# Performance work log

Measured on AMD Instinct MI355X. Metric: run time of the kernel, lower is better.

Reference implementation:

```python
import jax, jax.numpy as jnp
import numpy as np

INPUT_DIM, DIM_K, DIM_V = 1024, 512, 512

def setup_inputs() -> dict:
    key = jax.random.key(0)
    kx, kq, kk, kv = jax.random.split(key, 4)
    x = jax.random.normal(kx, (4, 4096, INPUT_DIM), dtype=jnp.float32)
    s = 1.0 / np.sqrt(INPUT_DIM)
    Wq = jax.random.normal(kq, (INPUT_DIM, DIM_K), dtype=jnp.float32) * s
    Wk = jax.random.normal(kk, (INPUT_DIM, DIM_K), dtype=jnp.float32) * s
    Wv = jax.random.normal(kv, (INPUT_DIM, DIM_V), dtype=jnp.float32) * s
    return {"x": x, "Wq": Wq, "Wk": Wk, "Wv": Wv}

def reference(x, Wq, Wk, Wv):
    # x: [b, n, d_in]; bias-free projections
    Q = jnp.einsum('bnd,dk->bnk', x, Wq)
    K = jnp.einsum('bnd,dk->bnk', x, Wk)
    V = jnp.einsum('bnd,dv->bnv', x, Wv)
    scale = 1.0 / np.sqrt(Wq.shape[1])
    scores = jnp.einsum('bqk,bnk->bqn', Q, K) * scale  # [b, n, n]
    atten = jax.nn.softmax(scores, axis=-1)
    return jnp.einsum('bqn,bnv->bqv', atten, V)
```

## Files before the change

kernel.cpp:

```cpp
#include <hip/hip_runtime.h>
#include <hip/hip_bf16.h>


typedef __attribute__((ext_vector_type(8))) short bf16x8;
typedef __attribute__((ext_vector_type(4))) float floatx4;

static __device__ __forceinline__ unsigned short f2bf(float f) {
    unsigned int u = __builtin_bit_cast(unsigned int, f);
    return (unsigned short)((u + 0x7fffu + ((u >> 16) & 1u)) >> 16);
}

static __device__ __forceinline__ void gl2lds16(const unsigned short* g, unsigned short* l) {
    __builtin_amdgcn_global_load_lds(
        (const __attribute__((address_space(1))) unsigned int*)g,
        (__attribute__((address_space(3))) unsigned int*)l, 16, 0, 0);
}

__global__ __launch_bounds__(256) void cvt_bf16(const float* __restrict__ X,
                                                unsigned short* __restrict__ Y, int n4) {
    int i = blockIdx.x * 256 + threadIdx.x;
    if (i < n4) {
        float4 v = reinterpret_cast<const float4*>(X)[i];
        ushort4 o;
        o.x = f2bf(v.x); o.y = f2bf(v.y); o.z = f2bf(v.z); o.w = f2bf(v.w);
        reinterpret_cast<ushort4*>(Y)[i] = o;
    }
}

__global__ __launch_bounds__(256) void transpose_w(const float* __restrict__ W,
                                                   unsigned short* __restrict__ Wt) {
    __shared__ float tile[32][33];
    int n0 = blockIdx.x * 32;
    int k0 = blockIdx.y * 32;
    int tx = threadIdx.x & 31, ty = threadIdx.x >> 5;
    for (int i = 0; i < 32; i += 8)
        tile[ty + i][tx] = W[(size_t)(k0 + ty + i) * 512 + n0 + tx];
    __syncthreads();
    for (int i = 0; i < 32; i += 8)
        Wt[(size_t)(n0 + ty + i) * 1024 + k0 + tx] = f2bf(tile[tx][ty + i]);
}

template <int MODE>
__global__ __launch_bounds__(256) void gemm_bt(const unsigned short* __restrict__ A,
                                               const unsigned short* __restrict__ Bt,
                                               unsigned short* __restrict__ C,
                                               int M, int N, int K) {
    __shared__ unsigned short As[128 * 32];
    __shared__ unsigned short Bs[128 * 32];
    const int m0 = blockIdx.y * 128, n0 = blockIdx.x * 128;
    const int tid = threadIdx.x;
    const int lane = tid & 63, wave = tid >> 6;
    const int wm = (wave >> 1) * 64, wn = (wave & 1) * 64;
    const int quad = lane >> 4, l15 = lane & 15;

    floatx4 acc[4][4] = {};
    const int srow = tid >> 2, scol = (tid & 3) * 8;

    for (int kt = 0; kt < K; kt += 32) {
        const unsigned short* ga = A + (size_t)(m0 + srow) * K + kt + scol;
        const unsigned short* gb = Bt + (size_t)(n0 + srow) * K + kt + scol;
        gl2lds16(ga, As + tid * 8);
        gl2lds16(ga + (size_t)64 * K, As + 2048 + tid * 8);
        gl2lds16(gb, Bs + tid * 8);
        gl2lds16(gb + (size_t)64 * K, Bs + 2048 + tid * 8);
        __syncthreads();
        bf16x8 af[4], bfr[4];
#pragma unroll
        for (int i = 0; i < 4; i++)
            af[i] = *reinterpret_cast<const bf16x8*>(As + (wm + i * 16 + l15) * 32 + quad * 8);
#pragma unroll
        for (int j = 0; j < 4; j++)
            bfr[j] = *reinterpret_cast<const bf16x8*>(Bs + (wn + j * 16 + l15) * 32 + quad * 8);
#pragma unroll
        for (int i = 0; i < 4; i++)
#pragma unroll
            for (int j = 0; j < 4; j++)
                acc[i][j] = __builtin_amdgcn_mfma_f32_16x16x32_bf16(af[i], bfr[j], acc[i][j], 0, 0, 0);
        __syncthreads();
    }

    const float qscale = 0.044194173824159216f;
#pragma unroll
    for (int i = 0; i < 4; i++)
#pragma unroll
        for (int j = 0; j < 4; j++)
#pragma unroll
            for (int r = 0; r < 4; r++) {
                int row = m0 + wm + i * 16 + quad * 4 + r;
                int col = n0 + wn + j * 16 + l15;
                float val = (MODE == 0) ? acc[i][j][r] * qscale : acc[i][j][r];
                unsigned short v = f2bf(val);
                if (MODE == 0) {
                    C[(size_t)row * N + col] = v;
                } else if (MODE == 1) {
                    size_t base = ((size_t)((row >> 12) * 128 + ((row & 4095) >> 5))) << 14;
                    int off = ((col >> 5) * 2 + ((row >> 4) & 1)) * 512 +
                              (((col >> 3) & 3) * 16 + (row & 15)) * 8 + (col & 7);
                    C[base + off] = v;
                } else {
                    size_t base = ((size_t)((col >> 12) * 128 + ((col & 4095) >> 5))) << 14;
                    int off = (row >> 4) * 512 +
                              (((col >> 3) & 3) * 16 + (row & 15)) * 8 + (col & 7);
                    C[base + off] = v;
                }
            }
}

__global__ __launch_bounds__(256, 2) void attn(const unsigned short* __restrict__ Qg,
                                               const unsigned short* __restrict__ Kf,
                                               const unsigned short* __restrict__ Vf,
                                               float* __restrict__ O0,
                                               float* __restrict__ O1,
                                               float* __restrict__ lpart) {
    __shared__ unsigned short Kb[16384];
    __shared__ unsigned short Vb[16384];
    __shared__ unsigned short Ps[4][512];

    const int b = blockIdx.y;
    const int q0 = blockIdx.x * 64;
    const int h = blockIdx.z;
    const int tid = threadIdx.x;
    const int lane = tid & 63, wave = tid >> 6;
    const int quad = lane >> 4, l15 = lane & 15;

    const unsigned short* KfB = Kf + ((size_t)b << 21);
    const unsigned short* VfB = Vf + ((size_t)b << 21);
    float* Od = (h == 0) ? O0 : O1;

    bf16x8 qf[16];
    {
        const unsigned short* qrow =
            Qg + (size_t)(b * 4096 + q0 + wave * 16 + l15) * 512 + quad * 8;
#pragma unroll
        for (int ks = 0; ks < 16; ks++)
            qf[ks] = *reinterpret_cast<const bf16x8*>(qrow + ks * 32);
    }

    floatx4 o[4][8];
#pragma unroll
    for (int g = 0; g < 4; g++)
#pragma unroll
        for (int n2 = 0; n2 < 8; n2++) o[g][n2] = floatx4{0.f, 0.f, 0.f, 0.f};
    float lp[4] = {0.f, 0.f, 0.f, 0.f};

    const int kt0 = h * 64;
    for (int kt = kt0; kt < kt0 + 64; kt++) {
        const unsigned short* gK = KfB + ((size_t)kt << 14);
        const unsigned short* gV = VfB + ((size_t)kt << 14);
#pragma unroll
        for (int i = 0; i < 8; i++)
            gl2lds16(gK + (i * 256 + tid) * 8, &Kb[(i * 256 + tid) * 8]);
#pragma unroll
        for (int i = 0; i < 8; i++)
            gl2lds16(gV + (i * 256 + tid) * 8, &Vb[(i * 256 + tid) * 8]);
        __syncthreads();

        floatx4 s00 = {0.f,0.f,0.f,0.f}, s01 = {0.f,0.f,0.f,0.f};
        floatx4 s10 = {0.f,0.f,0.f,0.f}, s11 = {0.f,0.f,0.f,0.f};
#pragma unroll
        for (int ks = 0; ks < 16; ks += 2) {
            bf16x8 k0a = *reinterpret_cast<const bf16x8*>(Kb + (2 * ks + 0) * 512 + lane * 8);
            bf16x8 k1a = *reinterpret_cast<const bf16x8*>(Kb + (2 * ks + 1) * 512 + lane * 8);
            bf16x8 k0b = *reinterpret_cast<const bf16x8*>(Kb + (2 * ks + 2) * 512 + lane * 8);
            bf16x8 k1b = *reinterpret_cast<const bf16x8*>(Kb + (2 * ks + 3) * 512 + lane * 8);
            s00 = __builtin_amdgcn_mfma_f32_16x16x32_bf16(qf[ks], k0a, s00, 0, 0, 0);
            s10 = __builtin_amdgcn_mfma_f32_16x16x32_bf16(qf[ks], k1a, s10, 0, 0, 0);
            s01 = __builtin_amdgcn_mfma_f32_16x16x32_bf16(qf[ks + 1], k0b, s01, 0, 0, 0);
            s11 = __builtin_amdgcn_mfma_f32_16x16x32_bf16(qf[ks + 1], k1b, s11, 0, 0, 0);
        }
        floatx4 s0v = s00 + s01, s1v = s10 + s11;

        unsigned short* Pw = &Ps[wave][0];
#pragma unroll
        for (int r = 0; r < 4; r++) {
            float p0 = __expf(s0v[r] - 16.0f);
            float p1 = __expf(s1v[r] - 16.0f);
            lp[r] += p0 + p1;
            int row = quad * 4 + r;
            Pw[(l15 >> 3) * 128 + row * 8 + (l15 & 7)] = f2bf(p0);
            Pw[((l15 >> 3) + 2) * 128 + row * 8 + (l15 & 7)] = f2bf(p1);
        }
        __syncthreads();

        bf16x8 vfr[8];
#pragma unroll
        for (int n2 = 0; n2 < 8; n2++)
            vfr[n2] = *reinterpret_cast<const bf16x8*>(Vb + (wave * 8 + n2) * 512 + lane * 8);
#pragma unroll
        for (int g = 0; g < 4; g++) {
            bf16x8 pf = *reinterpret_cast<const bf16x8*>(&Ps[g][0] + lane * 8);
#pragma unroll
            for (int n2 = 0; n2 < 8; n2++)
                o[g][n2] = __builtin_amdgcn_mfma_f32_16x16x32_bf16(pf, vfr[n2], o[g][n2], 0, 0, 0);
        }
        __syncthreads();
    }

#pragma unroll
    for (int off = 1; off < 16; off <<= 1)
#pragma unroll
        for (int r = 0; r < 4; r++) lp[r] += __shfl_xor(lp[r], off);
    if (l15 == 0) {
#pragma unroll
        for (int r = 0; r < 4; r++)
            lpart[h * 16384 + b * 4096 + q0 + wave * 16 + quad * 4 + r] = lp[r];
    }

#pragma unroll
    for (int g = 0; g < 4; g++)
#pragma unroll
        for (int r = 0; r < 4; r++) {
            size_t rowoff = (size_t)(b * 4096 + q0 + g * 16 + quad * 4 + r) * 512 + wave * 128 + l15;
#pragma unroll
            for (int n2 = 0; n2 < 8; n2++)
                Od[rowoff + n2 * 16] = o[g][n2][r];
        }
}

__global__ __launch_bounds__(256) void combine(float* __restrict__ Out,
                                               const float* __restrict__ O1,
                                               const float* __restrict__ lpart) {
    int i = blockIdx.x * 256 + threadIdx.x;
    int row = i >> 7;
    float inv = 1.0f / (lpart[row] + lpart[16384 + row]);
    float4 a = reinterpret_cast<const float4*>(Out)[i];
    float4 c = reinterpret_cast<const float4*>(O1)[i];
    float4 r;
    r.x = (a.x + c.x) * inv;
    r.y = (a.y + c.y) * inv;
    r.z = (a.z + c.z) * inv;
    r.w = (a.w + c.w) * inv;
    reinterpret_cast<float4*>(Out)[i] = r;
}

extern "C" void kernel_launch(void* const* d_in, const int* in_sizes, int n_in,
                              void* d_out, int out_size, void* d_ws, size_t ws_size,
                              hipStream_t stream) {
    const float* x  = (const float*)d_in[0];
    const float* Wq = (const float*)d_in[1];
    const float* Wk = (const float*)d_in[2];
    const float* Wv = (const float*)d_in[3];

    char* ws = (char*)d_ws;
    unsigned short* Wqt = (unsigned short*)(ws);
    unsigned short* Wkt = (unsigned short*)(ws + (1u << 20));
    unsigned short* Wvt = (unsigned short*)(ws + (2u << 20));
    unsigned short* Qb  = (unsigned short*)(ws + (3u << 20));
    unsigned short* Kfr = (unsigned short*)(ws + (19u << 20));
    unsigned short* Vfr = (unsigned short*)(ws + (35u << 20));
    unsigned short* xb  = (unsigned short*)(ws + (51u << 20));
    float* O1    = (float*)(ws + (51u << 20));
    float* lpart = (float*)(ws + (83u << 20));

    dim3 tb(256);
    cvt_bf16<<<dim3(16384), tb, 0, stream>>>(x, xb, 16384 * 1024 / 4);
    transpose_w<<<dim3(16, 32), tb, 0, stream>>>(Wq, Wqt);
    transpose_w<<<dim3(16, 32), tb, 0, stream>>>(Wk, Wkt);
    transpose_w<<<dim3(16, 32), tb, 0, stream>>>(Wv, Wvt);
    gemm_bt<0><<<dim3(4, 128), tb, 0, stream>>>(xb, Wqt, Qb, 16384, 512, 1024);
    gemm_bt<1><<<dim3(4, 128), tb, 0, stream>>>(xb, Wkt, Kfr, 16384, 512, 1024);
    gemm_bt<2><<<dim3(128, 4), tb, 0, stream>>>(Wvt, xb, Vfr, 512, 16384, 1024);
    attn<<<dim3(64, 4, 2), tb, 0, stream>>>(Qb, Kfr, Vfr, (float*)d_out, O1, lpart);
    combine<<<dim3(8192), tb, 0, stream>>>((float*)d_out, O1, lpart);
}
```

Baseline: 373.3 us.

## Fuse QKV projections into one GEMM and double-buffer attention K/V tiles

The three projection GEMMs are merged into a single launch over a concatenated transposed weight, and each block writes Q, K-fragment or V-fragment layout depending on its column range. V is now produced in the non-transposed orientation with a recomputed fragment index. The attention kernel grows to 512 threads covering 128 queries, with two query halves sharing each K/V tile, and double-buffers K/V in LDS using async loads with explicit vmcnt waits and raw barriers so the next tile's load overlaps current compute. This roughly doubles LDS use per block, which may limit occupancy, and the hand-written waitcnt counts are fragile. It also issues one redundant wrapped prefetch on the last iteration.

```diff
diff --git a/kernel.cpp b/kernel.cpp
--- a/kernel.cpp
+++ b/kernel.cpp
@@ -15,6 +15,12 @@
         (const __attribute__((address_space(1))) unsigned int*)g,
         (__attribute__((address_space(3))) unsigned int*)l, 16, 0, 0);
 }
+
+#define BAR() __asm__ volatile("s_barrier" ::: "memory")
+#define WVMC12() __asm__ volatile("s_waitcnt vmcnt(12)" ::: "memory")
+#define WVMC8() __asm__ volatile("s_waitcnt vmcnt(8)" ::: "memory")
+#define WLGKM0() __asm__ volatile("s_waitcnt lgkmcnt(0)" ::: "memory")
+#define WALL() __asm__ volatile("s_waitcnt vmcnt(0) lgkmcnt(0)" ::: "memory")
 
 __global__ __launch_bounds__(256) void cvt_bf16(const float* __restrict__ X,
                                                 unsigned short* __restrict__ Y, int n4) {
@@ -28,7 +34,7 @@
 }
 
 __global__ __launch_bounds__(256) void transpose_w(const float* __restrict__ W,
-                                                   unsigned short* __restrict__ Wt) {
+                                                   unsigned short* __restrict__ Wt, int off) {
     __shared__ float tile[32][33];
     int n0 = blockIdx.x * 32;
     int k0 = blockIdx.y * 32;
@@ -37,16 +43,17 @@
         tile[ty + i][tx] = W[(size_t)(k0 + ty + i) * 512 + n0 + tx];
     __syncthreads();
     for (int i = 0; i < 32; i += 8)
-        Wt[(size_t)(n0 + ty + i) * 1024 + k0 + tx] = f2bf(tile[tx][ty + i]);
-}
-
-template <int MODE>
-__global__ __launch_bounds__(256) void gemm_bt(const unsigned short* __restrict__ A,
-                                               const unsigned short* __restrict__ Bt,
-                                               unsigned short* __restrict__ C,
-                                               int M, int N, int K) {
+        Wt[(size_t)(off + n0 + ty + i) * 1024 + k0 + tx] = f2bf(tile[tx][ty + i]);
+}
+
+__global__ __launch_bounds__(256) void gemm_qkv(const unsigned short* __restrict__ A,
+                                                const unsigned short* __restrict__ Bt,
+                                                unsigned short* __restrict__ Qb,
+                                                unsigned short* __restrict__ Kfr,
+                                                unsigned short* __restrict__ Vfr) {
     __shared__ unsigned short As[128 * 32];
     __shared__ unsigned short Bs[128 * 32];
+    const int K = 1024;
     const int m0 = blockIdx.y * 128, n0 = blockIdx.x * 128;
     const int tid = threadIdx.x;
     const int lane = tid & 63, wave = tid >> 6;
@@ -88,40 +95,41 @@
             for (int r = 0; r < 4; r++) {
                 int row = m0 + wm + i * 16 + quad * 4 + r;
                 int col = n0 + wn + j * 16 + l15;
-                float val = (MODE == 0) ? acc[i][j][r] * qscale : acc[i][j][r];
-                unsigned short v = f2bf(val);
-                if (MODE == 0) {
-                    C[(size_t)row * N + col] = v;
-                } else if (MODE == 1) {
+                if (n0 < 512) {
+                    Qb[(size_t)row * 512 + col] = f2bf(acc[i][j][r] * qscale);
+                } else if (n0 < 1024) {
+                    int d = col - 512;
                     size_t base = ((size_t)((row >> 12) * 128 + ((row & 4095) >> 5))) << 14;
-                    int off = ((col >> 5) * 2 + ((row >> 4) & 1)) * 512 +
-                              (((col >> 3) & 3) * 16 + (row & 15)) * 8 + (col & 7);
-                    C[base + off] = v;
+                    int off = ((d >> 5) * 2 + ((row >> 4) & 1)) * 512 +
+                              (((d >> 3) & 3) * 16 + (row & 15)) * 8 + (d & 7);
+                    Kfr[base + off] = f2bf(acc[i][j][r]);
                 } else {
-                    size_t base = ((size_t)((col >> 12) * 128 + ((col & 4095) >> 5))) << 14;
-                    int off = (row >> 4) * 512 +
-                              (((col >> 3) & 3) * 16 + (row & 15)) * 8 + (col & 7);
-                    C[base + off] = v;
+                    int d = col - 1024;
+                    size_t base = ((size_t)((row >> 12) * 128 + ((row & 4095) >> 5))) << 14;
+                    int off = (d >> 4) * 512 +
+                              (((row & 31) >> 3) * 16 + (d & 15)) * 8 + (row & 7);
+                    Vfr[base + off] = f2bf(acc[i][j][r]);
                 }
             }
 }
 
-__global__ __launch_bounds__(256, 2) void attn(const unsigned short* __restrict__ Qg,
+__global__ __launch_bounds__(512, 2) void attn(const unsigned short* __restrict__ Qg,
                                                const unsigned short* __restrict__ Kf,
                                                const unsigned short* __restrict__ Vf,
                                                float* __restrict__ O0,
                                                float* __restrict__ O1,
                                                float* __restrict__ lpart) {
-    __shared__ unsigned short Kb[16384];
-    __shared__ unsigned short Vb[16384];
-    __shared__ unsigned short Ps[4][512];
+    __shared__ unsigned short Kb[2][16384];
+    __shared__ unsigned short Vb[2][16384];
+    __shared__ unsigned short Ps[8][512];
 
     const int b = blockIdx.y;
-    const int q0 = blockIdx.x * 64;
+    const int q0 = blockIdx.x * 128;
     const int h = blockIdx.z;
     const int tid = threadIdx.x;
     const int lane = tid & 63, wave = tid >> 6;
     const int quad = lane >> 4, l15 = lane & 15;
+    const int qh = wave >> 2, dq = wave & 3;
 
     const unsigned short* KfB = Kf + ((size_t)b << 21);
     const unsigned short* VfB = Vf + ((size_t)b << 21);
@@ -135,6 +143,7 @@
         for (int ks = 0; ks < 16; ks++)
             qf[ks] = *reinterpret_cast<const bf16x8*>(qrow + ks * 32);
     }
+    WALL();
 
     floatx4 o[4][8];
 #pragma unroll
@@ -144,25 +153,42 @@
     float lp[4] = {0.f, 0.f, 0.f, 0.f};
 
     const int kt0 = h * 64;
-    for (int kt = kt0; kt < kt0 + 64; kt++) {
-        const unsigned short* gK = KfB + ((size_t)kt << 14);
-        const unsigned short* gV = VfB + ((size_t)kt << 14);
-#pragma unroll
-        for (int i = 0; i < 8; i++)
-            gl2lds16(gK + (i * 256 + tid) * 8, &Kb[(i * 256 + tid) * 8]);
-#pragma unroll
-        for (int i = 0; i < 8; i++)
-            gl2lds16(gV + (i * 256 + tid) * 8, &Vb[(i * 256 + tid) * 8]);
-        __syncthreads();
-
+    {
+        const unsigned short* gK = KfB + ((size_t)kt0 << 14);
+        const unsigned short* gV = VfB + ((size_t)kt0 << 14);
+#pragma unroll
+        for (int i = 0; i < 4; i++)
+            gl2lds16(gK + (i * 512 + tid) * 8, &Kb[0][(i * 512 + tid) * 8]);
+#pragma unroll
+        for (int i = 0; i < 4; i++)
+            gl2lds16(gV + (i * 512 + tid) * 8, &Vb[0][(i * 512 + tid) * 8]);
+    }
+
+    for (int it = 0; it < 64; it++) {
+        const int cur = it & 1, nxt = cur ^ 1;
+        const int ktn = kt0 + ((it + 1) & 63);
+        {
+            const unsigned short* gK = KfB + ((size_t)ktn << 14);
+            const unsigned short* gV = VfB + ((size_t)ktn << 14);
+#pragma unroll
+            for (int i = 0; i < 4; i++)
+                gl2lds16(gK + (i * 512 + tid) * 8, &Kb[nxt][(i * 512 + tid) * 8]);
+#pragma unroll
+            for (int i = 0; i < 4; i++)
+                gl2lds16(gV + (i * 512 + tid) * 8, &Vb[nxt][(i * 512 + tid) * 8]);
+        }
+        WVMC12();
+        BAR();
+
+        const unsigned short* Kc = &Kb[cur][0];
         floatx4 s00 = {0.f,0.f,0.f,0.f}, s01 = {0.f,0.f,0.f,0.f};
         floatx4 s10 = {0.f,0.f,0.f,0.f}, s11 = {0.f,0.f,0.f,0.f};
 #pragma unroll
         for (int ks = 0; ks < 16; ks += 2) {
-            bf16x8 k0a = *reinterpret_cast<const bf16x8*>(Kb + (2 * ks + 0) * 512 + lane * 8);
-            bf16x8 k1a = *reinterpret_cast<const bf16x8*>(Kb + (2 * ks + 1) * 512 + lane * 8);
-            bf16x8 k0b = *reinterpret_cast<const bf16x8*>(Kb + (2 * ks + 2) * 512 + lane * 8);
-            bf16x8 k1b = *reinterpret_cast<const bf16x8*>(Kb + (2 * ks + 3) * 512 + lane * 8);
+            bf16x8 k0a = *reinterpret_cast<const bf16x8*>(Kc + (2 * ks + 0) * 512 + lane * 8);
+            bf16x8 k1a = *reinterpret_cast<const bf16x8*>(Kc + (2 * ks + 1) * 512 + lane * 8);
+            bf16x8 k0b = *reinterpret_cast<const bf16x8*>(Kc + (2 * ks + 2) * 512 + lane * 8);
+            bf16x8 k1b = *reinterpret_cast<const bf16x8*>(Kc + (2 * ks + 3) * 512 + lane * 8);
             s00 = __builtin_amdgcn_mfma_f32_16x16x32_bf16(qf[ks], k0a, s00, 0, 0, 0);
             s10 = __builtin_amdgcn_mfma_f32_16x16x32_bf16(qf[ks], k1a, s10, 0, 0, 0);
             s01 = __builtin_amdgcn_mfma_f32_16x16x32_bf16(qf[ks + 1], k0b, s01, 0, 0, 0);
@@ -180,21 +206,25 @@
             Pw[(l15 >> 3) * 128 + row * 8 + (l15 & 7)] = f2bf(p0);
             Pw[((l15 >> 3) + 2) * 128 + row * 8 + (l15 & 7)] = f2bf(p1);
         }
-        __syncthreads();
-
+        WLGKM0();
+        WVMC8();
+        BAR();
+
+        const unsigned short* Vc = &Vb[cur][0];
         bf16x8 vfr[8];
 #pragma unroll
         for (int n2 = 0; n2 < 8; n2++)
-            vfr[n2] = *reinterpret_cast<const bf16x8*>(Vb + (wave * 8 + n2) * 512 + lane * 8);
+            vfr[n2] = *reinterpret_cast<const bf16x8*>(Vc + (dq * 8 + n2) * 512 + lane * 8);
 #pragma unroll
         for (int g = 0; g < 4; g++) {
-            bf16x8 pf = *reinterpret_cast<const bf16x8*>(&Ps[g][0] + lane * 8);
+            bf16x8 pf = *reinterpret_cast<const bf16x8*>(&Ps[qh * 4 + g][0] + lane * 8);
 #pragma unroll
             for (int n2 = 0; n2 < 8; n2++)
                 o[g][n2] = __builtin_amdgcn_mfma_f32_16x16x32_bf16(pf, vfr[n2], o[g][n2], 0, 0, 0);
         }
-        __syncthreads();
-    }
+        BAR();
+    }
+    WALL();
 
 #pragma unroll
     for (int off = 1; off < 16; off <<= 1)
@@ -210,7 +240,8 @@
     for (int g = 0; g < 4; g++)
 #pragma unroll
         for (int r = 0; r < 4; r++) {
-            size_t rowoff = (size_t)(b * 4096 + q0 + g * 16 + quad * 4 + r) * 512 + wave * 128 + l15;
+            size_t rowoff = (size_t)(b * 4096 + q0 + qh * 64 + g * 16 + quad * 4 + r) * 512
+                            + dq * 128 + l15;
 #pragma unroll
             for (int n2 = 0; n2 < 8; n2++)
                 Od[rowoff + n2 * 16] = o[g][n2][r];
@@ -242,9 +273,7 @@
     const float* Wv = (const float*)d_in[3];
 
     char* ws = (char*)d_ws;
-    unsigned short* Wqt = (unsigned short*)(ws);
-    unsigned short* Wkt = (unsigned short*)(ws + (1u << 20));
-    unsigned short* Wvt = (unsigned short*)(ws + (2u << 20));
+    unsigned short* Wtall = (unsigned short*)(ws);
     unsigned short* Qb  = (unsigned short*)(ws + (3u << 20));
     unsigned short* Kfr = (unsigned short*)(ws + (19u << 20));
     unsigned short* Vfr = (unsigned short*)(ws + (35u << 20));
@@ -254,12 +283,10 @@
 
     dim3 tb(256);
     cvt_bf16<<<dim3(16384), tb, 0, stream>>>(x, xb, 16384 * 1024 / 4);
-    transpose_w<<<dim3(16, 32), tb, 0, stream>>>(Wq, Wqt);
-    transpose_w<<<dim3(16, 32), tb, 0, stream>>>(Wk, Wkt);
-    transpose_w<<<dim3(16, 32), tb, 0, stream>>>(Wv, Wvt);
-    gemm_bt<0><<<dim3(4, 128), tb, 0, stream>>>(xb, Wqt, Qb, 16384, 512, 1024);
-    gemm_bt<1><<<dim3(4, 128), tb, 0, stream>>>(xb, Wkt, Kfr, 16384, 512, 1024);
-    gemm_bt<2><<<dim3(128, 4), tb, 0, stream>>>(Wvt, xb, Vfr, 512, 16384, 1024);
-    attn<<<dim3(64, 4, 2), tb, 0, stream>>>(Qb, Kfr, Vfr, (float*)d_out, O1, lpart);
+    transpose_w<<<dim3(16, 32), tb, 0, stream>>>(Wq, Wtall, 0);
+    transpose_w<<<dim3(16, 32), tb, 0, stream>>>(Wk, Wtall, 512);
+    transpose_w<<<dim3(16, 32), tb, 0, stream>>>(Wv, Wtall, 1024);
+    gemm_qkv<<<dim3(12, 128), tb, 0, stream>>>(xb, Wtall, Qb, Kfr, Vfr);
+    attn<<<dim3(32, 4, 2), dim3(512), 0, stream>>>(Qb, Kfr, Vfr, (float*)d_out, O1, lpart);
     combine<<<dim3(8192), tb, 0, stream>>>((float*)d_out, O1, lpart);
 }
```

After: 362.3 us. -3.0%, faster.
